# Kernel tuning notes

Hardware: AMD Instinct MI355X
Metric: run time of the kernel (lower is better)

## Reference

```python
import jax, jax.numpy as jnp
import numpy as np

DIM = 1024
NUM_HEADS = 16
HEAD_DIM = DIM // NUM_HEADS


def setup_inputs() -> dict:
    key = jax.random.key(0)
    ks = jax.random.split(key, 9)
    s = 1.0 / np.sqrt(DIM)
    x = jax.random.normal(ks[0], (2, 2048, DIM), dtype=jnp.float32)
    Wq = jax.random.uniform(ks[1], (DIM, DIM), jnp.float32, -s, s)
    bq = jax.random.uniform(ks[2], (DIM,), jnp.float32, -s, s)
    Wk = jax.random.uniform(ks[3], (DIM, DIM), jnp.float32, -s, s)
    bk = jax.random.uniform(ks[4], (DIM,), jnp.float32, -s, s)
    Wv = jax.random.uniform(ks[5], (DIM, DIM), jnp.float32, -s, s)
    bv = jax.random.uniform(ks[6], (DIM,), jnp.float32, -s, s)
    Wo = jax.random.uniform(ks[7], (DIM, DIM), jnp.float32, -s, s)
    bo = jax.random.uniform(ks[8], (DIM,), jnp.float32, -s, s)
    return {"x": x, "Wq": Wq, "bq": bq, "Wk": Wk, "bk": bk,
            "Wv": Wv, "bv": bv, "Wo": Wo, "bo": bo}


def reference(x, Wq, bq, Wk, bk, Wv, bv, Wo, bo):
    B, S, _ = x.shape
    # projections (torch Linear: y = x @ W.T + b); split heads -> [B, H, S, Dh]
    def split(y):
        return y.reshape(B, S, NUM_HEADS, HEAD_DIM).transpose(0, 2, 1, 3)
    q = split(x @ Wq.T + bq)
    k = split(x @ Wk.T + bk)
    v = split(x @ Wv.T + bv)
    scale = 1.0 / np.sqrt(HEAD_DIM).astype(np.float32)
    scores = jnp.einsum('bhqd,bhkd->bhqk', q, k) * scale  # [B,H,S,S]
    attn = jax.nn.softmax(scores, axis=-1)
    ctx = jnp.einsum('bhqk,bhkd->bhqd', attn, v)  # [B,H,S,Dh]
    ctx = ctx.transpose(0, 2, 1, 3).reshape(B, S, DIM)
    return ctx @ Wo.T + bo
```

## Files before the change

### kernel.cpp

```cpp
#include <hip/hip_runtime.h>
#include <hip/hip_bf16.h>
#include <math.h>

#define DIMSZ 1024
#define NHEAD 16
#define HDIM 64
#define BATCH 2
#define SEQ 2048
#define NROWS (BATCH * SEQ)

#define QSCALE 0.18033688011112042592f

typedef __attribute__((ext_vector_type(8))) short bf16x8;
typedef __attribute__((ext_vector_type(4))) float f32x4;

__device__ __forceinline__ int swz(int m) { return (m ^ (m >> 2)) & 3; }

__device__ __forceinline__ unsigned hipack(unsigned a, unsigned b) {
    return __builtin_amdgcn_perm(b, a, 0x07060302u);
}

__device__ __forceinline__ void cvt2(float x, float y, unsigned& h, unsigned& l) {
    unsigned ux = __float_as_uint(x), uy = __float_as_uint(y);
    h = hipack(ux, uy);
    float rx = x - __uint_as_float(ux & 0xFFFF0000u);
    float ry = y - __uint_as_float(uy & 0xFFFF0000u);
    l = hipack(__float_as_uint(rx), __float_as_uint(ry));
}

__device__ __forceinline__ void cvt8(const float4& f0, const float4& f1,
                                     uint4& hv, uint4& lv) {
    cvt2(f0.x, f0.y, hv.x, lv.x);
    cvt2(f0.z, f0.w, hv.y, lv.y);
    cvt2(f1.x, f1.y, hv.z, lv.z);
    cvt2(f1.z, f1.w, hv.w, lv.w);
}

__device__ __forceinline__ ushort f2bf(float x) {
    union { __hip_bfloat16 b; ushort u; } cv;
    cv.b = __float2bfloat16(x);
    return cv.u;
}

__device__ __forceinline__ void gld16(const void* g, void* l) {
    __builtin_amdgcn_global_load_lds((const __attribute__((address_space(1))) void*)g,
                                     (__attribute__((address_space(3))) void*)l,
                                     16, 0, 0);
}

__global__ __launch_bounds__(256) void convert_all(
    const float* __restrict__ x,
    const float* __restrict__ Wq, const float* __restrict__ Wk,
    const float* __restrict__ Wv, const float* __restrict__ Wo,
    ushort* __restrict__ Xhi,
    ushort* __restrict__ Whi, ushort* __restrict__ Wlo,
    ushort* __restrict__ Wohi)
{
    const int b = blockIdx.x;
    const float* src;
    ushort* hi;
    ushort* lo = nullptr;
    size_t off;
    if (b < 2048)      { src = x;  hi = Xhi;  off = (size_t)b * 2048; }
    else if (b < 2560) { src = Wq; hi = Whi;             lo = Wlo;             off = (size_t)(b - 2048) * 2048; }
    else if (b < 3072) { src = Wk; hi = Whi + (1 << 20); lo = Wlo + (1 << 20); off = (size_t)(b - 2560) * 2048; }
    else if (b < 3584) { src = Wv; hi = Whi + 2 * (1 << 20); lo = Wlo + 2 * (1 << 20); off = (size_t)(b - 3072) * 2048; }
    else               { src = Wo; hi = Wohi; off = (size_t)(b - 3584) * 2048; }

    const size_t i = off + (size_t)threadIdx.x * 8;
    const float4 f0 = *(const float4*)&src[i];
    const float4 f1 = *(const float4*)&src[i + 4];
    if (lo) {
        uint4 hv, lv;
        cvt8(f0, f1, hv, lv);
        *(uint4*)&hi[i] = hv;
        *(uint4*)&lo[i] = lv;
    } else {
        uint4 hv;
        hv.x = (unsigned)f2bf(f0.x) | ((unsigned)f2bf(f0.y) << 16);
        hv.y = (unsigned)f2bf(f0.z) | ((unsigned)f2bf(f0.w) << 16);
        hv.z = (unsigned)f2bf(f1.x) | ((unsigned)f2bf(f1.y) << 16);
        hv.w = (unsigned)f2bf(f1.z) | ((unsigned)f2bf(f1.w) << 16);
        *(uint4*)&hi[i] = hv;
    }
}

__global__ __launch_bounds__(256, 3) void qkv_gemm(
    const ushort* __restrict__ Xhi,
    const ushort* __restrict__ Whi, const ushort* __restrict__ Wlo,
    const float* __restrict__ bq, const float* __restrict__ bk,
    const float* __restrict__ bv,
    ushort* __restrict__ Qb, ushort* __restrict__ Kb, ushort* __restrict__ Vt)
{
    __shared__ __align__(16) ushort smem[17408];

    const int tid = threadIdx.x;
    const int wave = tid >> 6;
    const int lane = tid & 63;
    const int lm = lane & 15;
    const int lq = lane >> 4;
    const int wy = wave >> 1;
    const int wx = wave & 1;
    const int m0 = blockIdx.x * 128;
    const int nbase = blockIdx.y * 128;

    const int c = tid & 3;
    const int r0 = tid >> 2;
    const int g = c ^ swz(r0 & 15);
    const ushort* gah = Xhi + (size_t)(m0 + r0) * DIMSZ + g * 8;
    const ushort* gbh = Whi + (size_t)(nbase + r0) * DIMSZ + g * 8;
    const ushort* gbl = Wlo + (size_t)(nbase + r0) * DIMSZ + g * 8;
    const int wofs = wave * 512;

    const int fo = lm * 32 + (((lq ^ swz(lm)) & 3) << 3);
    int aofs[4], bofs[4];
#pragma unroll
    for (int i = 0; i < 4; ++i) {
        aofs[i] = (wy * 64 + i * 16) * 32 + fo;
        bofs[i] = (wx * 64 + i * 16) * 32 + fo;
    }

    f32x4 acc[4][4] = {};

    {
        gld16(gah, smem + wofs);                 gld16(gah + 64 * DIMSZ, smem + 2048 + wofs);
        gld16(gbh, smem + 4096 + wofs);          gld16(gbh + 64 * DIMSZ, smem + 6144 + wofs);
        gld16(gbl, smem + 8192 + wofs);          gld16(gbl + 64 * DIMSZ, smem + 10240 + wofs);
    }

    for (int kk = 0; kk < 32; ++kk) {
        __syncthreads();

        const ushort* Ah = smem;
        const ushort* Bh = smem + 4096;
        const ushort* Bl = smem + 8192;

        bf16x8 ahf[4], bhf[4], blf[4];
#pragma unroll
        for (int i = 0; i < 4; ++i) {
            ahf[i] = *(const bf16x8*)&Ah[aofs[i]];
            bhf[i] = *(const bf16x8*)&Bh[bofs[i]];
            blf[i] = *(const bf16x8*)&Bl[bofs[i]];
        }

        __syncthreads();

        if (kk + 1 < 32) {
            const int k0 = (kk + 1) * 32;
            gld16(gah + k0, smem + wofs);                 gld16(gah + 64 * DIMSZ + k0, smem + 2048 + wofs);
            gld16(gbh + k0, smem + 4096 + wofs);          gld16(gbh + 64 * DIMSZ + k0, smem + 6144 + wofs);
            gld16(gbl + k0, smem + 8192 + wofs);          gld16(gbl + 64 * DIMSZ + k0, smem + 10240 + wofs);
        }

#pragma unroll
        for (int i = 0; i < 4; ++i)
#pragma unroll
            for (int j = 0; j < 4; ++j) {
                acc[i][j] = __builtin_amdgcn_mfma_f32_16x16x32_bf16(ahf[i], bhf[j], acc[i][j], 0, 0, 0);
                acc[i][j] = __builtin_amdgcn_mfma_f32_16x16x32_bf16(ahf[i], blf[j], acc[i][j], 0, 0, 0);
            }
    }

    const int mat = blockIdx.y >> 3;
    const float* bias = (mat == 0) ? bq : (mat == 1) ? bk : bv;
    const int nloc0 = (blockIdx.y & 7) * 128;
    const int b = m0 >> 11;
    const int s0 = m0 & (SEQ - 1);
    ushort* sf = smem;

    __syncthreads();

    if (mat == 2) {
#pragma unroll
        for (int j = 0; j < 4; ++j) {
            const int nc = nloc0 + wx * 64 + j * 16 + lm;
            const float bb = bias[nc];
            const int d = j * 16 + lm;
#pragma unroll
            for (int i = 0; i < 4; ++i) {
                const int ss = wy * 64 + (i >> 1) * 32 + lq * 8 + (i & 1) * 4;
                ushort4 pk;
                pk.x = f2bf(acc[i][j][0] + bb);
                pk.y = f2bf(acc[i][j][1] + bb);
                pk.z = f2bf(acc[i][j][2] + bb);
                pk.w = f2bf(acc[i][j][3] + bb);
                *(ushort4*)&sf[(wx * 64 + d) * 136 + ss] = pk;
            }
        }
        __syncthreads();
#pragma unroll
        for (int p = 0; p < 8; ++p) {
            const int idx = p * 256 + tid;
            const int row = idx >> 4;
            const int hh = row >> 6;
            const int d = row & 63;
            const int sseg = (idx & 15) * 8;
            const uint4 v = *(const uint4*)&sf[row * 136 + sseg];
            const int hg = (nloc0 >> 6) + hh;
            *(uint4*)&Vt[((size_t)(b * NHEAD + hg) * HDIM + d) * SEQ + s0 + sseg] = v;
        }
    } else {
        ushort* dst = (mat == 0) ? Qb : Kb;
        const float sc = (mat == 0) ? QSCALE : 1.0f;
#pragma unroll
        for (int j = 0; j < 4; ++j) {
            const int col = wx * 64 + j * 16 + lm;
            const float bb = bias[nloc0 + col];
#pragma unroll
            for (int i = 0; i < 4; ++i) {
                const int rbase = wy * 64 + i * 16 + lq * 4;
#pragma unroll
                for (int rr = 0; rr < 4; ++rr)
                    sf[(rbase + rr) * 136 + col] = f2bf((acc[i][j][rr] + bb) * sc);
            }
        }
        __syncthreads();
#pragma unroll
        for (int p = 0; p < 8; ++p) {
            const int idx = p * 256 + tid;
            const int row = idx >> 4;
            const int seg = idx & 15;
            const uint4 v = *(const uint4*)&sf[row * 136 + seg * 8];
            const int nc0 = nloc0 + seg * 8;
            const int h = nc0 >> 6;
            const int d = nc0 & 63;
            *(uint4*)&dst[((size_t)(b * NHEAD + h) * SEQ + s0 + row) * HDIM + d] = v;
        }
    }
}

__global__ __launch_bounds__(256) void flash_attn_mfma(
    const ushort* __restrict__ Qb, const ushort* __restrict__ Kb,
    const ushort* __restrict__ Vt, ushort* __restrict__ CTXhi)
{
    __shared__ __align__(16) ushort Ks[2][4096];
    __shared__ __align__(16) ushort Vs[2][4096];

    const int tid = threadIdx.x;
    const int w = tid >> 6;
    const int l = tid & 63;
    const int lm = l & 15;
    const int lq = l >> 4;
    const int q0 = blockIdx.x * 128;
    const int bh = blockIdx.y;

    const ushort* Kg = Kb + (size_t)bh * SEQ * HDIM;
    const ushort* Vg = Vt + (size_t)bh * HDIM * SEQ;

    const int srow = w * 8 + (l >> 3);
    const int sc_ = (l & 7) ^ ((l >> 3) & 7);

    bf16x8 qf[2][2];
#pragma unroll
    for (int rt = 0; rt < 2; ++rt)
#pragma unroll
        for (int kt = 0; kt < 2; ++kt)
            qf[rt][kt] = *(const bf16x8*)&Qb[((size_t)bh * SEQ + q0 + w * 32 + rt * 16 + lm) * HDIM + kt * 32 + lq * 8];

    int koff[4][2];
#pragma unroll
    for (int t = 0; t < 4; ++t)
#pragma unroll
        for (int kt = 0; kt < 2; ++kt)
            koff[t][kt] = (t * 16 + lm) * 64 + (((kt * 4 + lq) ^ (lm & 7)) << 3);

    f32x4 o[2][4] = {};
    float l_[2] = {0.0f, 0.0f};

    {
        ushort* kb = &Ks[0][0];
        ushort* vb = &Vs[0][0];
#pragma unroll
        for (int p = 0; p < 2; ++p) {
            const int row = p * 32 + srow;
            gld16(Kg + (size_t)row * HDIM + sc_ * 8, kb + (p * 32 + w * 8) * 64);
            gld16(Vg + (size_t)row * SEQ + sc_ * 8, vb + (p * 32 + w * 8) * 64);
        }
    }

    for (int ch = 0; ch < SEQ / 64; ++ch) {
        __syncthreads();

        if (ch + 1 < SEQ / 64) {
            const int kc = (ch + 1) * 64;
            ushort* kb = &Ks[(ch + 1) & 1][0];
            ushort* vb = &Vs[(ch + 1) & 1][0];
#pragma unroll
            for (int p = 0; p < 2; ++p) {
                const int row = p * 32 + srow;
                gld16(Kg + (size_t)(kc + row) * HDIM + sc_ * 8, kb + (p * 32 + w * 8) * 64);
                gld16(Vg + (size_t)row * SEQ + kc + sc_ * 8, vb + (p * 32 + w * 8) * 64);
            }
        }

        const ushort* kb = &Ks[ch & 1][0];
        const ushort* vb = &Vs[ch & 1][0];

        f32x4 st[2][4] = {};
#pragma unroll
        for (int ct = 0; ct < 4; ++ct)
#pragma unroll
            for (int kt = 0; kt < 2; ++kt) {
                const bf16x8 kf = *(const bf16x8*)&kb[koff[ct][kt]];
#pragma unroll
                for (int rt = 0; rt < 2; ++rt)
                    st[rt][ct] = __builtin_amdgcn_mfma_f32_16x16x32_bf16(kf, qf[rt][kt], st[rt][ct], 0, 0, 0);
            }

#pragma unroll
        for (int rt = 0; rt < 2; ++rt) {
            float ls = 0.0f;
#pragma unroll
            for (int ct = 0; ct < 4; ++ct)
#pragma unroll
                for (int r = 0; r < 4; ++r) {
                    const float p = __builtin_amdgcn_exp2f(st[rt][ct][r]);
                    st[rt][ct][r] = p;
                    ls += p;
                }
            ls += __shfl_xor(ls, 16, 64);
            ls += __shfl_xor(ls, 32, 64);
            l_[rt] += ls;
        }

        bf16x8 pf[2][2];
#pragma unroll
        for (int rt = 0; rt < 2; ++rt)
#pragma unroll
            for (int kt2 = 0; kt2 < 2; ++kt2) {
                union { bf16x8 v; ushort u[8]; } pk;
#pragma unroll
                for (int t = 0; t < 2; ++t)
#pragma unroll
                    for (int r = 0; r < 4; ++r)
                        pk.u[t * 4 + r] = f2bf(st[rt][kt2 * 2 + t][r]);
                pf[rt][kt2] = pk.v;
            }

#pragma unroll
        for (int dt = 0; dt < 4; ++dt)
#pragma unroll
            for (int kt2 = 0; kt2 < 2; ++kt2) {
                const bf16x8 vf = *(const bf16x8*)&vb[koff[dt][kt2]];
#pragma unroll
                for (int rt = 0; rt < 2; ++rt)
                    o[rt][dt] = __builtin_amdgcn_mfma_f32_16x16x32_bf16(pf[rt][kt2], vf, o[rt][dt], 0, 0, 0);
            }
    }

    const int b = bh >> 4;
    const int h = bh & 15;
#pragma unroll
    for (int rt = 0; rt < 2; ++rt) {
        const float linv_me = 1.0f / l_[rt];
#pragma unroll
        for (int r = 0; r < 4; ++r) {
            const float lr = __shfl(linv_me, lq * 4 + r, 64);
            const int srow_ = q0 + w * 32 + rt * 16 + lq * 4 + r;
            const size_t base = ((size_t)b * SEQ + srow_) * DIMSZ + h * HDIM;
#pragma unroll
            for (int dt = 0; dt < 4; ++dt)
                CTXhi[base + dt * 16 + lm] = f2bf(o[rt][dt][r] * lr);
        }
    }
}

__global__ __launch_bounds__(256) void oproj_gemm(
    const ushort* __restrict__ Ahi_g, const ushort* __restrict__ Bhi_g,
    const float* __restrict__ bias, float* __restrict__ out)
{
    __shared__ __align__(16) ushort smem[6144];

    const int tid = threadIdx.x;
    const int wave = tid >> 6;
    const int lane = tid & 63;
    const int lm = lane & 15;
    const int lq = lane >> 4;
    const int wy = wave >> 1;
    const int wx = wave & 1;
    const int m0 = blockIdx.x * 64;
    const int n0 = blockIdx.y * 128;

    const int c = tid & 3;
    const int r0 = tid >> 2;
    const int g = c ^ swz(r0 & 15);
    const ushort* gah = Ahi_g + (size_t)(m0 + r0) * DIMSZ + g * 8;
    const ushort* gbh = Bhi_g + (size_t)(n0 + r0) * DIMSZ + g * 8;
    const int wofs = wave * 512;

    const int fo = lm * 32 + (((lq ^ swz(lm)) & 3) << 3);
    int aofs[2], bofs[4];
#pragma unroll
    for (int i = 0; i < 2; ++i) aofs[i] = (wy * 32 + i * 16) * 32 + fo;
#pragma unroll
    for (int j = 0; j < 4; ++j) bofs[j] = (wx * 64 + j * 16) * 32 + fo;

    f32x4 acc[2][4] = {};

    {
        gld16(gah, smem + wofs);
        gld16(gbh, smem + 2048 + wofs);   gld16(gbh + 64 * DIMSZ, smem + 4096 + wofs);
    }

    for (int kk = 0; kk < 32; ++kk) {
        __syncthreads();

        bf16x8 ahf[2], bhf[4];
#pragma unroll
        for (int i = 0; i < 2; ++i) ahf[i] = *(const bf16x8*)&smem[aofs[i]];
#pragma unroll
        for (int j = 0; j < 4; ++j) bhf[j] = *(const bf16x8*)&smem[2048 + bofs[j]];

        __syncthreads();

        if (kk + 1 < 32) {
            const int k0 = (kk + 1) * 32;
            gld16(gah + k0, smem + wofs);
            gld16(gbh + k0, smem + 2048 + wofs);   gld16(gbh + 64 * DIMSZ + k0, smem + 4096 + wofs);
        }

#pragma unroll
        for (int i = 0; i < 2; ++i)
#pragma unroll
            for (int j = 0; j < 4; ++j)
                acc[i][j] = __builtin_amdgcn_mfma_f32_16x16x32_bf16(ahf[i], bhf[j], acc[i][j], 0, 0, 0);
    }

#pragma unroll
    for (int j = 0; j < 4; ++j) {
        const int nc = n0 + wx * 64 + j * 16 + lm;
        const float bb = bias[nc];
#pragma unroll
        for (int i = 0; i < 2; ++i) {
            const int mb = m0 + wy * 32 + i * 16 + lq * 4;
#pragma unroll
            for (int rr = 0; rr < 4; ++rr)
                out[(size_t)(mb + rr) * DIMSZ + nc] = acc[i][j][rr] + bb;
        }
    }
}

extern "C" void kernel_launch(void* const* d_in, const int* in_sizes, int n_in,
                              void* d_out, int out_size, void* d_ws, size_t ws_size,
                              hipStream_t stream)
{
    const float* x  = (const float*)d_in[0];
    const float* Wq = (const float*)d_in[1];
    const float* bq = (const float*)d_in[2];
    const float* Wk = (const float*)d_in[3];
    const float* bk = (const float*)d_in[4];
    const float* Wv = (const float*)d_in[5];
    const float* bv = (const float*)d_in[6];
    const float* Wo = (const float*)d_in[7];
    const float* bo = (const float*)d_in[8];
    float* out = (float*)d_out;

    const size_t elems = (size_t)NROWS * DIMSZ;
    ushort* Qb    = (ushort*)d_ws;
    ushort* Kb    = Qb + elems;
    ushort* Vt    = Kb + elems;
    ushort* CTXhi = Vt + elems;
    ushort* Whi   = CTXhi + elems;
    ushort* Wlo   = Whi + 3 * (1 << 20);
    ushort* Wohi  = Wlo + 3 * (1 << 20);
    ushort* Xhi   = CTXhi;

    convert_all<<<4096, 256, 0, stream>>>(x, Wq, Wk, Wv, Wo,
                                          Xhi, Whi, Wlo, Wohi);

    qkv_gemm<<<dim3(32, 24), 256, 0, stream>>>(Xhi, Whi, Wlo, bq, bk, bv, Qb, Kb, Vt);

    flash_attn_mfma<<<dim3(SEQ / 128, BATCH * NHEAD), 256, 0, stream>>>(Qb, Kb, Vt, CTXhi);

    oproj_gemm<<<dim3(64, 8), 256, 0, stream>>>(CTXhi, Wohi, bo, out);
}
```

Baseline: 212.0 us.

## Split flash-attention query tile across 8 waves with 16 rows each

The attention kernel now runs 512 threads (8 waves) per block instead of 256. Each wave handles 16 query rows instead of 32, so per-wave registers and MFMA work are halved, and each wave stages a single K/V row group into shared memory instead of two. The aim is more waves in flight to hide LDS and exp latency. In exchange, each K/V fragment read from LDS now feeds one MFMA instead of two, so LDS read traffic per MFMA doubles, and block-wide barriers now synchronise more waves.

Result: faster. 203.6 us (-3.9%).

```diff
diff --git a/kernel.cpp b/kernel.cpp
--- a/kernel.cpp
+++ b/kernel.cpp
@@ -229,7 +229,7 @@
     }
 }
 
-__global__ __launch_bounds__(256) void flash_attn_mfma(
+__global__ __launch_bounds__(512, 4) void flash_attn_mfma(
     const ushort* __restrict__ Qb, const ushort* __restrict__ Kb,
     const ushort* __restrict__ Vt, ushort* __restrict__ CTXhi)
 {
@@ -250,12 +250,10 @@
     const int srow = w * 8 + (l >> 3);
     const int sc_ = (l & 7) ^ ((l >> 3) & 7);
 
-    bf16x8 qf[2][2];
-#pragma unroll
-    for (int rt = 0; rt < 2; ++rt)
-#pragma unroll
-        for (int kt = 0; kt < 2; ++kt)
-            qf[rt][kt] = *(const bf16x8*)&Qb[((size_t)bh * SEQ + q0 + w * 32 + rt * 16 + lm) * HDIM + kt * 32 + lq * 8];
+    bf16x8 qf[2];
+#pragma unroll
+    for (int kt = 0; kt < 2; ++kt)
+        qf[kt] = *(const bf16x8*)&Qb[((size_t)bh * SEQ + q0 + w * 16 + lm) * HDIM + kt * 32 + lq * 8];
 
     int koff[4][2];
 #pragma unroll
@@ -264,104 +262,82 @@
         for (int kt = 0; kt < 2; ++kt)
             koff[t][kt] = (t * 16 + lm) * 64 + (((kt * 4 + lq) ^ (lm & 7)) << 3);
 
-    f32x4 o[2][4] = {};
-    float l_[2] = {0.0f, 0.0f};
-
-    {
-        ushort* kb = &Ks[0][0];
-        ushort* vb = &Vs[0][0];
-#pragma unroll
-        for (int p = 0; p < 2; ++p) {
-            const int row = p * 32 + srow;
-            gld16(Kg + (size_t)row * HDIM + sc_ * 8, kb + (p * 32 + w * 8) * 64);
-            gld16(Vg + (size_t)row * SEQ + sc_ * 8, vb + (p * 32 + w * 8) * 64);
-        }
-    }
+    f32x4 o[4] = {};
+    float l_ = 0.0f;
+
+    gld16(Kg + (size_t)srow * HDIM + sc_ * 8, &Ks[0][0] + w * 8 * 64);
+    gld16(Vg + (size_t)srow * SEQ + sc_ * 8, &Vs[0][0] + w * 8 * 64);
 
     for (int ch = 0; ch < SEQ / 64; ++ch) {
         __syncthreads();
 
         if (ch + 1 < SEQ / 64) {
             const int kc = (ch + 1) * 64;
-            ushort* kb = &Ks[(ch + 1) & 1][0];
-            ushort* vb = &Vs[(ch + 1) & 1][0];
-#pragma unroll
-            for (int p = 0; p < 2; ++p) {
-                const int row = p * 32 + srow;
-                gld16(Kg + (size_t)(kc + row) * HDIM + sc_ * 8, kb + (p * 32 + w * 8) * 64);
-                gld16(Vg + (size_t)row * SEQ + kc + sc_ * 8, vb + (p * 32 + w * 8) * 64);
-            }
+            ushort* kb_n = &Ks[(ch + 1) & 1][0];
+            ushort* vb_n = &Vs[(ch + 1) & 1][0];
+            gld16(Kg + (size_t)(kc + srow) * HDIM + sc_ * 8, kb_n + w * 8 * 64);
+            gld16(Vg + (size_t)srow * SEQ + kc + sc_ * 8, vb_n + w * 8 * 64);
         }
 
         const ushort* kb = &Ks[ch & 1][0];
         const ushort* vb = &Vs[ch & 1][0];
 
-        f32x4 st[2][4] = {};
+        f32x4 st[4] = {};
 #pragma unroll
         for (int ct = 0; ct < 4; ++ct)
 #pragma unroll
             for (int kt = 0; kt < 2; ++kt) {
                 const bf16x8 kf = *(const bf16x8*)&kb[koff[ct][kt]];
-#pragma unroll
-                for (int rt = 0; rt < 2; ++rt)
-                    st[rt][ct] = __builtin_amdgcn_mfma_f32_16x16x32_bf16(kf, qf[rt][kt], st[rt][ct], 0, 0, 0);
+                st[ct] = __builtin_amdgcn_mfma_f32_16x16x32_bf16(kf, qf[kt], st[ct], 0, 0, 0);
             }
 
-#pragma unroll
-        for (int rt = 0; rt < 2; ++rt) {
+        {
             float ls = 0.0f;
 #pragma unroll
             for (int ct = 0; ct < 4; ++ct)
 #pragma unroll
                 for (int r = 0; r < 4; ++r) {
-                    const float p = __builtin_amdgcn_exp2f(st[rt][ct][r]);
-                    st[rt][ct][r] = p;
+                    const float p = __builtin_amdgcn_exp2f(st[ct][r]);
+                    st[ct][r] = p;
                     ls += p;
                 }
             ls += __shfl_xor(ls, 16, 64);
             ls += __shfl_xor(ls, 32, 64);
-            l_[rt] += ls;
-        }
-
-        bf16x8 pf[2][2];
-#pragma unroll
-        for (int rt = 0; rt < 2; ++rt)
-#pragma unroll
-            for (int kt2 = 0; kt2 < 2; ++kt2) {
-                union { bf16x8 v; ushort u[8]; } pk;
-#pragma unroll
-                for (int t = 0; t < 2; ++t)
-#pragma unroll
-                    for (int r = 0; r < 4; ++r)
-                        pk.u[t * 4 + r] = f2bf(st[rt][kt2 * 2 + t][r]);
-                pf[rt][kt2] = pk.v;
-            }
+            l_ += ls;
+        }
+
+        bf16x8 pf[2];
+#pragma unroll
+        for (int kt2 = 0; kt2 < 2; ++kt2) {
+            union { bf16x8 v; ushort u[8]; } pk;
+#pragma unroll
+            for (int t = 0; t < 2; ++t)
+#pragma unroll
+                for (int r = 0; r < 4; ++r)
+                    pk.u[t * 4 + r] = f2bf(st[kt2 * 2 + t][r]);
+            pf[kt2] = pk.v;
+        }
 
 #pragma unroll
         for (int dt = 0; dt < 4; ++dt)
 #pragma unroll
             for (int kt2 = 0; kt2 < 2; ++kt2) {
                 const bf16x8 vf = *(const bf16x8*)&vb[koff[dt][kt2]];
-#pragma unroll
-                for (int rt = 0; rt < 2; ++rt)
-                    o[rt][dt] = __builtin_amdgcn_mfma_f32_16x16x32_bf16(pf[rt][kt2], vf, o[rt][dt], 0, 0, 0);
+                o[dt] = __builtin_amdgcn_mfma_f32_16x16x32_bf16(pf[kt2], vf, o[dt], 0, 0, 0);
             }
     }
 
     const int b = bh >> 4;
     const int h = bh & 15;
-#pragma unroll
-    for (int rt = 0; rt < 2; ++rt) {
-        const float linv_me = 1.0f / l_[rt];
-#pragma unroll
-        for (int r = 0; r < 4; ++r) {
-            const float lr = __shfl(linv_me, lq * 4 + r, 64);
-            const int srow_ = q0 + w * 32 + rt * 16 + lq * 4 + r;
-            const size_t base = ((size_t)b * SEQ + srow_) * DIMSZ + h * HDIM;
-#pragma unroll
-            for (int dt = 0; dt < 4; ++dt)
-                CTXhi[base + dt * 16 + lm] = f2bf(o[rt][dt][r] * lr);
-        }
+    const float linv_me = 1.0f / l_;
+#pragma unroll
+    for (int r = 0; r < 4; ++r) {
+        const float lr = __shfl(linv_me, lq * 4 + r, 64);
+        const int srow_ = q0 + w * 16 + lq * 4 + r;
+        const size_t base = ((size_t)b * SEQ + srow_) * DIMSZ + h * HDIM;
+#pragma unroll
+        for (int dt = 0; dt < 4; ++dt)
+            CTXhi[base + dt * 16 + lm] = f2bf(o[dt][r] * lr);
     }
 }
 
@@ -470,7 +446,7 @@
 
     qkv_gemm<<<dim3(32, 24), 256, 0, stream>>>(Xhi, Whi, Wlo, bq, bk, bv, Qb, Kb, Vt);
 
-    flash_attn_mfma<<<dim3(SEQ / 128, BATCH * NHEAD), 256, 0, stream>>>(Qb, Kb, Vt, CTXhi);
+    flash_attn_mfma<<<dim3(SEQ / 128, BATCH * NHEAD), 512, 0, stream>>>(Qb, Kb, Vt, CTXhi);
 
     oproj_gemm<<<dim3(64, 8), 256, 0, stream>>>(CTXhi, Wohi, bo, out);
 }
```
